# Kernel tuning notes

Hardware: AMD Instinct MI355X
Metric: run time of the kernel (lower is better)

The kernel has to match this reference:

```python
import jax, jax.numpy as jnp
import numpy as np

B, S, HID, H = 8, 128, 256, 4
DH = HID // H
FF = 4 * HID


def setup_inputs() -> dict:
    key = jax.random.key(0)
    ks = jax.random.split(key, 16)
    n = lambda i, shape: jax.random.normal(ks[i], shape, dtype=jnp.float32) * 0.02
    z = lambda shape: jnp.zeros(shape, dtype=jnp.float32)
    return dict(
        x=jax.random.normal(ks[0], (B, S, HID), dtype=jnp.float32),
        attention_mask=jnp.zeros((B, 1, S, S), dtype=jnp.float32),
        Wq=n(1, (HID, HID)), bq=z((HID,)),
        Wk=n(2, (HID, HID)), bk=z((HID,)),
        Wv=n(3, (HID, HID)), bv=z((HID,)),
        order_w=n(4, (2 * DH,)), order_b=z(()),
        dist_w=n(5, (2 * DH,)), dist_b=z(()),
        scalar=jax.random.normal(ks[6], (1,), dtype=jnp.float32),
        AWq=n(7, (HID, HID)), Abq=z((HID,)),
        AWk=n(8, (HID, HID)), Abk=z((HID,)),
        Wd=n(9, (HID, HID)), bd=z((HID,)),
        g1=jnp.ones((HID,), jnp.float32), beta1=z((HID,)),
        W1=n(10, (HID, FF)), b1=z((FF,)),
        W2=n(11, (FF, HID)), b2=z((HID,)),
        g2=jnp.ones((HID,), jnp.float32), beta2=z((HID,)),
    )


def _ln(t, g, b, eps=1e-12):
    m = t.mean(-1, keepdims=True)
    v = ((t - m) ** 2).mean(-1, keepdims=True)
    return (t - m) / jnp.sqrt(v + eps) * g + b


def _heads(t):
    # [B,S,HID] -> [B,H,S,DH]
    return t.reshape(B, S, H, DH).transpose(0, 2, 1, 3)


def reference(x, attention_mask, Wq, bq, Wk, bk, Wv, bv, order_w, order_b,
              dist_w, dist_b, scalar, AWq, Abq, AWk, Abk, Wd, bd,
              g1, beta1, W1, b1, W2, b2, g2, beta2):
    inv = 1.0 / jnp.sqrt(jnp.float32(DH))
    q = x @ Wq + bq
    k = x @ Wk + bk
    v = x @ Wv + bv
    qh, kh, vh = _heads(q), _heads(k), _heads(v)
    scores = jnp.einsum('bhqd,bhkd->bhqk', qh, kh)  # [B,H,S,S]

    # order/distance affines on concat(q_i, k_j): Linear(2*DH,1) decomposes into
    # per-token projections summed via broadcast (same math, no [B,H,S,S,2*DH] tensor)
    pr_order = jax.nn.sigmoid((qh @ order_w[:DH])[..., :, None]
                              + (kh @ order_w[DH:])[..., None, :] + order_b)
    gd_order = jnp.triu(jnp.ones((S, S), jnp.float32), k=1)
    err_order = (jnp.log(pr_order + 1e-24) * gd_order
                 + jnp.log(1.0 - pr_order + 1e-24) * (1.0 - gd_order))

    idx = jnp.arange(S)
    gd_dist = jnp.log(jnp.abs(idx[None, :] - idx[:, None]).astype(jnp.float32) + 1.0)
    pr_dist = ((qh @ dist_w[:DH])[..., :, None]
               + (kh @ dist_w[DH:])[..., None, :] + dist_b)
    err_dist = -jnp.square(gd_dist - pr_dist) * jnp.square(scalar[0]) * 0.5

    rich_scores = scores + err_order + err_dist
    softm = lambda s: jax.nn.softmax(s * inv + attention_mask, axis=-1)
    rich_probs = softm(rich_scores)
    origin_probs = softm(scores)

    # rich/calibrated combine ('fixed'): softmax(origin + 0.5 * rich)
    combined = jax.nn.softmax(origin_probs + 0.5 * rich_probs, axis=-1)

    # two-level attack attention on transformed mixed q/k
    aq, ak = _heads(q @ AWq + Abq), _heads(k @ AWk + Abk)
    attack_probs = softm(jnp.einsum('bhqd,bhkd->bhqk', aq, ak))
    final_probs = jax.nn.softmax(combined + 0.5 * attack_probs, axis=-1)

    ctx = jnp.einsum('bhqk,bhkd->bhqd', final_probs, vh)
    ctx = ctx.transpose(0, 2, 1, 3).reshape(B, S, HID)
    h = _ln(ctx @ Wd + bd + x, g1, beta1)
    f = jax.nn.gelu(h @ W1 + b1, approximate=False) @ W2 + b2
    return _ln(f + h, g2, beta2)
```

## Files before the change

kernel.cpp:

```cpp
#include <hip/hip_runtime.h>
#include <hip/hip_bf16.h>
#include <math.h>

#define B_  8
#define S_  128
#define HID_ 256
#define H_  4
#define DH_ 64
#define FF_ 1024
#define M_  (B_ * S_)

typedef _Float16 half_t;
typedef __attribute__((ext_vector_type(8))) _Float16 half8;
typedef __attribute__((ext_vector_type(4))) float floatx4;

enum { EP_F32 = 0, EP_F16 = 1, EP_F16B = 2, EP_GELU = 3, EP_PROJ = 4 };

__device__ __forceinline__ floatx4 mfma16(half8 a, half8 b, floatx4 c) {
    return __builtin_amdgcn_mfma_f32_16x16x32_f16(a, b, c, 0, 0, 0);
}

__device__ __forceinline__ float wred_sum(float v) {
#pragma unroll
    for (int o = 32; o >= 1; o >>= 1) v += __shfl_xor(v, o, 64);
    return v;
}
__device__ __forceinline__ float block_sum_256(float v, float* s4, int tid) {
    v = wred_sum(v);
    __syncthreads();
    if ((tid & 63) == 0) s4[tid >> 6] = v;
    __syncthreads();
    return s4[0] + s4[1] + s4[2] + s4[3];
}
__device__ __forceinline__ float qred_sum(float v) {
#pragma unroll
    for (int o = 1; o < 16; o <<= 1) v += __shfl_xor(v, o, 64);
    return v;
}
__device__ __forceinline__ void sm8(float (&v)[8]) {
    float s = 0.f;
#pragma unroll
    for (int j = 0; j < 8; ++j) { v[j] = __expf(v[j]); s += v[j]; }
    s = qred_sum(s);
    float r = 1.f / s;
#pragma unroll
    for (int j = 0; j < 8; ++j) v[j] *= r;
}

template<int EPI>
__device__ __forceinline__ void mgemm(
    const half_t* __restrict__ A, int ldA,
    const half_t* __restrict__ Bt, int ldB,
    int kLen, int m0, int n0,
    const float* __restrict__ bias,
    float* __restrict__ Cf, half_t* __restrict__ Ch, int ldC,
    const float* __restrict__ pw1, const float* __restrict__ pw2,
    float* __restrict__ po1, float* __restrict__ po2, int hsel)
{
    __shared__ half8 Asf[2][4][64];
    __shared__ half8 Bsf[2][4][64];

    const int tid = threadIdx.x;
    const int w = tid >> 6, l = tid & 63;
    const int sr = tid >> 2;
    const int sq = tid & 3;
    const int sdst = (sr & 15) | (sq << 4);
    const int smt = sr >> 4;
    const half_t* Ap = A + (size_t)(m0 + sr) * ldA + sq * 8;
    const half_t* Bp = Bt + (size_t)(n0 + sr) * ldB + sq * 8;

    half8 ra, rb;
    auto fetch = [&](int t) {
        ra = *(const half8*)(Ap + t * 32);
        rb = *(const half8*)(Bp + t * 32);
    };
    auto commit = [&](int buf) {
        Asf[buf][smt][sdst] = ra;
        Bsf[buf][smt][sdst] = rb;
    };

    floatx4 zero = {0.f, 0.f, 0.f, 0.f};
    floatx4 acc[4] = {zero, zero, zero, zero};
    const int kt = kLen >> 5;

    fetch(0);
    commit(0);
    __syncthreads();
    for (int t = 0; t < kt; ++t) {
        const bool more = (t + 1 < kt);
        if (more) fetch(t + 1);
        const int buf = t & 1;
        half8 a = Asf[buf][w][l];
        acc[0] = mfma16(a, Bsf[buf][0][l], acc[0]);
        acc[1] = mfma16(a, Bsf[buf][1][l], acc[1]);
        acc[2] = mfma16(a, Bsf[buf][2][l], acc[2]);
        acc[3] = mfma16(a, Bsf[buf][3][l], acc[3]);
        if (more) {
            commit((t + 1) & 1);
            __syncthreads();
        }
    }

    const int quad = l >> 4, lc = l & 15;
    const int rowb = m0 + w * 16 + quad * 4;
    float bvv[4] = {0.f, 0.f, 0.f, 0.f};
    if (EPI >= EP_F16B) {
#pragma unroll
        for (int nt = 0; nt < 4; ++nt) bvv[nt] = bias[n0 + nt * 16 + lc];
    }
    float pw1v[4], pw2v[4];
    if (EPI == EP_PROJ) {
#pragma unroll
        for (int nt = 0; nt < 4; ++nt) {
            pw1v[nt] = pw1[nt * 16 + lc];
            pw2v[nt] = pw2[nt * 16 + lc];
        }
    }
#pragma unroll
    for (int rr = 0; rr < 4; ++rr) {
        float ov[4];
#pragma unroll
        for (int nt = 0; nt < 4; ++nt) {
            float o = acc[nt][rr];
            if (EPI >= EP_F16B) o += bvv[nt];
            if (EPI == EP_GELU) o = 0.5f * o * (1.f + erff(o * 0.70710678118654752f));
            ov[nt] = o;
            const size_t ci = (size_t)(rowb + rr) * ldC + n0 + nt * 16 + lc;
            if (EPI == EP_F32) Cf[ci] = o;
            else Ch[ci] = (half_t)o;
        }
        if (EPI == EP_PROJ) {
            float po = ov[0] * pw1v[0] + ov[1] * pw1v[1] + ov[2] * pw1v[2] + ov[3] * pw1v[3];
            float pd = ov[0] * pw2v[0] + ov[1] * pw2v[1] + ov[2] * pw2v[2] + ov[3] * pw2v[3];
#pragma unroll
            for (int off = 1; off < 16; off <<= 1) {
                po += __shfl_xor(po, off, 64);
                pd += __shfl_xor(pd, off, 64);
            }
            if (lc == 0) {
                const int m = rowb + rr;
                const int idx = ((m >> 7) * H_ + hsel) * S_ + (m & 127);
                po1[idx] = po;
                po2[idx] = pd;
            }
        }
    }
}

__global__ __launch_bounds__(256) void prep_kernel(
    const float* __restrict__ x,
    const float* __restrict__ Wq, const float* __restrict__ Wk,
    const float* __restrict__ Wv, const float* __restrict__ Wd,
    const float* __restrict__ AWq, const float* __restrict__ AWk,
    const float* __restrict__ W1, const float* __restrict__ W2,
    half_t* __restrict__ x16, half_t* __restrict__ Wq16n, half_t* __restrict__ Wk16n,
    half_t* __restrict__ WqT, half_t* __restrict__ WkT, half_t* __restrict__ WvT,
    half_t* __restrict__ WdT, half_t* __restrict__ AWqT, half_t* __restrict__ AWkT,
    half_t* __restrict__ W1T, half_t* __restrict__ W2T)
{
    const int z = blockIdx.z, bx = blockIdx.x, by = blockIdx.y;
    const int tid = threadIdx.x;
    if (z < 3) {
        const float* src = (z == 0) ? x : (z == 1) ? Wq : Wk;
        half_t* dst = (z == 0) ? x16 : (z == 1) ? Wq16n : Wk16n;
        const int total = (z == 0) ? M_ * HID_ : HID_ * HID_;
        const int bid = by * 16 + bx;
        if (bid * 1024 < total) {
            const int base = bid * 1024 + tid * 4;
            float4 vv = *(const float4*)(src + base);
            dst[base + 0] = (half_t)vv.x;
            dst[base + 1] = (half_t)vv.y;
            dst[base + 2] = (half_t)vv.z;
            dst[base + 3] = (half_t)vv.w;
        }
        return;
    }
    const float* src; half_t* dst; int K, N, k0, n0;
    if (z <= 8) {
        const float* ins[6] = {Wq, Wk, Wv, Wd, AWq, AWk};
        half_t* outs[6] = {WqT, WkT, WvT, WdT, AWqT, AWkT};
        src = ins[z - 3]; dst = outs[z - 3];
        K = 256; N = 256; k0 = bx * 64; n0 = by * 64;
        if (bx >= 4 || by >= 4) return;
    } else if (z == 9) {
        src = W1; dst = W1T; K = 256; N = 1024;
        k0 = bx * 64; n0 = by * 64;
        if (bx >= 4) return;
    } else {
        src = W2; dst = W2T; K = 1024; N = 256;
        k0 = by * 64; n0 = bx * 64;
        if (bx >= 4) return;
    }
    __shared__ half_t tl[64][72];
    const int r = tid >> 2, c0 = (tid & 3) * 16;
#pragma unroll 4
    for (int i = 0; i < 16; ++i)
        tl[c0 + i][r] = (half_t)src[(size_t)(k0 + r) * N + n0 + c0 + i];
    __syncthreads();
#pragma unroll 4
    for (int i = 0; i < 16; ++i)
        dst[(size_t)(n0 + r) * K + k0 + c0 + i] = tl[r][c0 + i];
}

__global__ __launch_bounds__(256) void compose_mfma(
    const half_t* __restrict__ AWqT, const half_t* __restrict__ AWkT,
    const half_t* __restrict__ Wq16n, const half_t* __restrict__ Wk16n,
    const float* __restrict__ AWq, const float* __restrict__ AWk,
    const float* __restrict__ bq, const float* __restrict__ bk,
    const float* __restrict__ Abq, const float* __restrict__ Abk,
    half_t* __restrict__ WcqT, half_t* __restrict__ WckT,
    float* __restrict__ bcq, float* __restrict__ bck)
{
    const int z = blockIdx.z;
    if (blockIdx.y < 4) {
        const half_t* A = z ? AWkT : AWqT;
        const half_t* Bt = z ? Wk16n : Wq16n;
        half_t* C = z ? WckT : WcqT;
        mgemm<EP_F16>(A, HID_, Bt, HID_, HID_, blockIdx.y * 64, blockIdx.x * 64,
                      nullptr, nullptr, C, HID_, nullptr, nullptr, nullptr, nullptr, 0);
    } else {
        __shared__ float red[4][64];
        const float* bsrc = z ? bk : bq;
        const float* AW   = z ? AWk : AWq;
        const float* Ab   = z ? Abk : Abq;
        float* bco        = z ? bck : bcq;
        int t = threadIdx.x, l = t & 63, kc = t >> 6;
        int n = blockIdx.x * 64 + l;
        float p = 0.f;
#pragma unroll 8
        for (int kk = 0; kk < 64; ++kk) {
            int k = kc * 64 + kk;
            p = fmaf(bsrc[k], AW[(size_t)k * HID_ + n], p);
        }
        red[kc][l] = p;
        __syncthreads();
        if (kc == 0)
            bco[n] = red[0][l] + red[1][l] + red[2][l] + red[3][l] + Ab[n];
    }
}

__global__ __launch_bounds__(256) void xgemm5(
    const half_t* __restrict__ x16,
    const half_t* __restrict__ WqT, const float* __restrict__ bq,
    const half_t* __restrict__ WkT, const float* __restrict__ bk,
    const half_t* __restrict__ WvT, const float* __restrict__ bv,
    const half_t* __restrict__ WcqT, const float* __restrict__ bcq,
    const half_t* __restrict__ WckT, const float* __restrict__ bck,
    const float* __restrict__ order_w, const float* __restrict__ dist_w,
    half_t* __restrict__ q16, half_t* __restrict__ k16, half_t* __restrict__ v16,
    half_t* __restrict__ aq16, half_t* __restrict__ ak16,
    float* __restrict__ qoA, float* __restrict__ qdA,
    float* __restrict__ koA, float* __restrict__ kdA)
{
    const int z = blockIdx.z;
    const int m0 = blockIdx.y * 64, n0 = blockIdx.x * 64;
    if (z == 0)
        mgemm<EP_PROJ>(x16, HID_, WqT, HID_, HID_, m0, n0, bq, nullptr, q16, HID_,
                       order_w, dist_w, qoA, qdA, blockIdx.x);
    else if (z == 1)
        mgemm<EP_PROJ>(x16, HID_, WkT, HID_, HID_, m0, n0, bk, nullptr, k16, HID_,
                       order_w + DH_, dist_w + DH_, koA, kdA, blockIdx.x);
    else if (z == 2)
        mgemm<EP_F16B>(x16, HID_, WvT, HID_, HID_, m0, n0, bv, nullptr, v16, HID_,
                       nullptr, nullptr, nullptr, nullptr, 0);
    else if (z == 3)
        mgemm<EP_F16B>(x16, HID_, WcqT, HID_, HID_, m0, n0, bcq, nullptr, aq16, HID_,
                       nullptr, nullptr, nullptr, nullptr, 0);
    else
        mgemm<EP_F16B>(x16, HID_, WckT, HID_, HID_, m0, n0, bck, nullptr, ak16, HID_,
                       nullptr, nullptr, nullptr, nullptr, 0);
}

__global__ __launch_bounds__(64) void attn_fused(
    const half_t* __restrict__ q16, const half_t* __restrict__ k16,
    const half_t* __restrict__ v16, const half_t* __restrict__ aq16,
    const half_t* __restrict__ ak16,
    const float* __restrict__ qoA, const float* __restrict__ qdA,
    const float* __restrict__ koA, const float* __restrict__ kdA,
    const float* __restrict__ mask,
    const float* __restrict__ order_b_p, const float* __restrict__ dist_b_p,
    const float* __restrict__ scalar_p,
    half_t* __restrict__ ctx16)
{
    __shared__ half8 Qf[2][64], AQf[2][64];
    __shared__ half8 Kf[2][8][64], AKf[2][8][64];
    __shared__ half_t Vt[64][136];
    __shared__ half_t Pm[16][136];

    const int l = threadIdx.x;
    const int quad = l >> 4, lc = l & 15;
    const int bh = blockIdx.x >> 3, rt = blockIdx.x & 7;
    const int b = bh >> 2, h = bh & 3;
    const size_t hoff = (size_t)b * S_ * HID_ + h * DH_;

#pragma unroll
    for (int u = 0; u < 2; ++u) {
        int idx = u * 64 + l;
        int r = idx >> 3, c = idx & 7;
        size_t g = hoff + (size_t)(rt * 16 + r) * HID_ + c * 8;
        int kt = c >> 2, sl = r | ((c & 3) << 4);
        Qf[kt][sl]  = *(const half8*)(q16 + g);
        AQf[kt][sl] = *(const half8*)(aq16 + g);
    }
#pragma unroll
    for (int u = 0; u < 16; ++u) {
        int idx = u * 64 + l;
        int j = idx >> 3, c = idx & 7;
        size_t g = hoff + (size_t)j * HID_ + c * 8;
        int kt = c >> 2, jt = j >> 4, sl = (j & 15) | ((c & 3) << 4);
        Kf[kt][jt][sl]  = *(const half8*)(k16 + g);
        AKf[kt][jt][sl] = *(const half8*)(ak16 + g);
    }
#pragma unroll
    for (int u = 0; u < 16; ++u) {
        int j = (u >> 3) * 64 + l;
        int c = u & 7;
        half8 vv = *(const half8*)(v16 + hoff + (size_t)j * HID_ + c * 8);
#pragma unroll
        for (int e = 0; e < 8; ++e) Vt[c * 8 + e][j] = vv[e];
    }
    __syncthreads();

    floatx4 zero = {0.f, 0.f, 0.f, 0.f};
    floatx4 accS[8], accA[8];
#pragma unroll
    for (int jt = 0; jt < 8; ++jt) { accS[jt] = zero; accA[jt] = zero; }
#pragma unroll
    for (int kt = 0; kt < 2; ++kt) {
        half8 a0 = Qf[kt][l];
        half8 a1 = AQf[kt][l];
#pragma unroll
        for (int jt = 0; jt < 8; ++jt) {
            accS[jt] = mfma16(a0, Kf[kt][jt][l], accS[jt]);
            accA[jt] = mfma16(a1, AKf[kt][jt][l], accA[jt]);
        }
    }

    const float ob = order_b_p[0], db = dist_b_p[0];
    const float scl = scalar_p[0];
    const float s2 = scl * scl;
    const float inv = 0.125f;
    float kov[8], kdv[8];
#pragma unroll
    for (int jt = 0; jt < 8; ++jt) {
        kov[jt] = koA[bh * S_ + jt * 16 + lc];
        kdv[jt] = kdA[bh * S_ + jt * 16 + lc];
    }
#pragma unroll
    for (int reg = 0; reg < 4; ++reg) {
        const int il = quad * 4 + reg;
        const int i  = rt * 16 + il;
        float qo = qoA[bh * S_ + i], qd = qdA[bh * S_ + i];
        const float* mrow = mask + ((size_t)(b * S_ + i)) * S_;
        float mk[8], lg[8], as_[8];
#pragma unroll
        for (int jt = 0; jt < 8; ++jt) {
            mk[jt] = mrow[jt * 16 + lc];
            lg[jt] = accS[jt][reg];
            as_[jt] = accA[jt][reg];
        }
        float p0[8];
#pragma unroll
        for (int jt = 0; jt < 8; ++jt) p0[jt] = lg[jt] * inv + mk[jt];
        sm8(p0);
        float p1[8];
#pragma unroll
        for (int jt = 0; jt < 8; ++jt) {
            int j = jt * 16 + lc;
            float pr = 1.f / (1.f + __expf(-(qo + kov[jt] + ob)));
            float sel = (j > i) ? pr : 1.f - pr;
            float erro = __logf(sel + 1e-24f);
            float gd = __logf(fabsf((float)(j - i)) + 1.f);
            float dd = gd - (qd + kdv[jt] + db);
            p1[jt] = (lg[jt] + erro - 0.5f * dd * dd * s2) * inv + mk[jt];
        }
        sm8(p1);
#pragma unroll
        for (int jt = 0; jt < 8; ++jt) p0[jt] += 0.5f * p1[jt];
        sm8(p0);
#pragma unroll
        for (int jt = 0; jt < 8; ++jt) p1[jt] = as_[jt] * inv + mk[jt];
        sm8(p1);
#pragma unroll
        for (int jt = 0; jt < 8; ++jt) p0[jt] += 0.5f * p1[jt];
        sm8(p0);
#pragma unroll
        for (int jt = 0; jt < 8; ++jt) Pm[il][jt * 16 + lc] = (half_t)p0[jt];
    }
    __syncthreads();

    half8 pa_[4];
#pragma unroll
    for (int kt = 0; kt < 4; ++kt)
        pa_[kt] = *(const half8*)&Pm[lc][kt * 32 + quad * 8];
    floatx4 apv[4];
#pragma unroll
    for (int nt = 0; nt < 4; ++nt) apv[nt] = zero;
#pragma unroll
    for (int nt = 0; nt < 4; ++nt) {
#pragma unroll
        for (int kt = 0; kt < 4; ++kt) {
            half8 vf = *(const half8*)&Vt[nt * 16 + lc][kt * 32 + quad * 8];
            apv[nt] = mfma16(pa_[kt], vf, apv[nt]);
        }
    }
#pragma unroll
    for (int nt = 0; nt < 4; ++nt) {
#pragma unroll
        for (int reg = 0; reg < 4; ++reg) {
            int i = rt * 16 + quad * 4 + reg;
            ctx16[hoff + (size_t)i * HID_ + nt * 16 + lc] = (half_t)apv[nt][reg];
        }
    }
}

__global__ __launch_bounds__(256) void dense_mfma(
    const half_t* __restrict__ ctx16, const half_t* __restrict__ WdT,
    float* __restrict__ dn)
{
    mgemm<EP_F32>(ctx16, HID_, WdT, HID_, HID_, blockIdx.y * 64, blockIdx.x * 64,
                  nullptr, dn, nullptr, HID_, nullptr, nullptr, nullptr, nullptr, 0);
}

__global__ __launch_bounds__(256) void ff1_mfma(
    const half_t* __restrict__ h16, const half_t* __restrict__ W1T,
    const float* __restrict__ b1, half_t* __restrict__ f116)
{
    mgemm<EP_GELU>(h16, HID_, W1T, HID_, HID_, blockIdx.y * 64, blockIdx.x * 64,
                   b1, nullptr, f116, FF_, nullptr, nullptr, nullptr, nullptr, 0);
}

__global__ __launch_bounds__(256) void ff2_mfma(
    const half_t* __restrict__ f116, const half_t* __restrict__ W2T,
    float* __restrict__ p0, float* __restrict__ p1,
    float* __restrict__ p2, float* __restrict__ p3)
{
    const int z = blockIdx.z;
    float* C = (z == 0) ? p0 : (z == 1) ? p1 : (z == 2) ? p2 : p3;
    mgemm<EP_F32>(f116 + z * 256, FF_, W2T + z * 256, FF_, 256,
                  blockIdx.y * 64, blockIdx.x * 64,
                  nullptr, C, nullptr, HID_, nullptr, nullptr, nullptr, nullptr, 0);
}

__global__ __launch_bounds__(256) void ln1_kernel(
    const float* __restrict__ dn, const float* __restrict__ bd,
    const float* __restrict__ x,
    const float* __restrict__ g1, const float* __restrict__ beta1,
    float* __restrict__ h32, half_t* __restrict__ h16)
{
    __shared__ float s4[4];
    const int row = blockIdx.x;
    const int n = threadIdx.x;
    const size_t idx = (size_t)row * HID_ + n;
    float val = dn[idx] + bd[n] + x[idx];
    float mean = block_sum_256(val, s4, n) * (1.f / HID_);
    float dv = val - mean;
    float var = block_sum_256(dv * dv, s4, n) * (1.f / HID_);
    float r = dv * rsqrtf(var + 1e-12f) * g1[n] + beta1[n];
    h32[idx] = r;
    h16[idx] = (half_t)r;
}

__global__ __launch_bounds__(256) void ln2_kernel(
    const float* __restrict__ p0, const float* __restrict__ p1,
    const float* __restrict__ p2, const float* __restrict__ p3,
    const float* __restrict__ b2, const float* __restrict__ h32,
    const float* __restrict__ g2, const float* __restrict__ beta2,
    float* __restrict__ out)
{
    __shared__ float s4[4];
    const int row = blockIdx.x;
    const int n = threadIdx.x;
    const size_t idx = (size_t)row * HID_ + n;
    float val = p0[idx] + p1[idx] + p2[idx] + p3[idx] + b2[n] + h32[idx];
    float mean = block_sum_256(val, s4, n) * (1.f / HID_);
    float dv = val - mean;
    float var = block_sum_256(dv * dv, s4, n) * (1.f / HID_);
    out[idx] = dv * rsqrtf(var + 1e-12f) * g2[n] + beta2[n];
}

extern "C" void kernel_launch(void* const* d_in, const int* in_sizes, int n_in,
                              void* d_out, int out_size, void* d_ws, size_t ws_size,
                              hipStream_t stream) {
    const float* x        = (const float*)d_in[0];
    const float* mask     = (const float*)d_in[1];
    const float* Wq       = (const float*)d_in[2];
    const float* bq       = (const float*)d_in[3];
    const float* Wk       = (const float*)d_in[4];
    const float* bk       = (const float*)d_in[5];
    const float* Wv       = (const float*)d_in[6];
    const float* bv       = (const float*)d_in[7];
    const float* order_w  = (const float*)d_in[8];
    const float* order_b  = (const float*)d_in[9];
    const float* dist_w   = (const float*)d_in[10];
    const float* dist_b   = (const float*)d_in[11];
    const float* scalar   = (const float*)d_in[12];
    const float* AWq      = (const float*)d_in[13];
    const float* Abq      = (const float*)d_in[14];
    const float* AWk      = (const float*)d_in[15];
    const float* Abk      = (const float*)d_in[16];
    const float* Wd       = (const float*)d_in[17];
    const float* bd       = (const float*)d_in[18];
    const float* g1       = (const float*)d_in[19];
    const float* beta1    = (const float*)d_in[20];
    const float* W1       = (const float*)d_in[21];
    const float* b1       = (const float*)d_in[22];
    const float* W2       = (const float*)d_in[23];
    const float* b2       = (const float*)d_in[24];
    const float* g2       = (const float*)d_in[25];
    const float* beta2    = (const float*)d_in[26];

    float* ws = (float*)d_ws;
    size_t off = 0;
    auto afl = [&](size_t n) { float* p = ws + off; off += n; return p; };
    auto ahf = [&](size_t nh) { half_t* p = (half_t*)(ws + off); off += nh / 2; return p; };

    half_t* x16   = ahf(M_ * HID_);
    half_t* Wq16n = ahf(HID_ * HID_);
    half_t* Wk16n = ahf(HID_ * HID_);
    half_t* WqT   = ahf(HID_ * HID_);
    half_t* WkT   = ahf(HID_ * HID_);
    half_t* WvT   = ahf(HID_ * HID_);
    half_t* WdT   = ahf(HID_ * HID_);
    half_t* AWqT  = ahf(HID_ * HID_);
    half_t* AWkT  = ahf(HID_ * HID_);
    half_t* W1T   = ahf(HID_ * FF_);
    half_t* W2T   = ahf(HID_ * FF_);
    half_t* WcqT  = ahf(HID_ * HID_);
    half_t* WckT  = ahf(HID_ * HID_);
    half_t* q16   = ahf(M_ * HID_);
    half_t* k16   = ahf(M_ * HID_);
    half_t* v16   = ahf(M_ * HID_);
    half_t* aq16  = ahf(M_ * HID_);
    half_t* ak16  = ahf(M_ * HID_);
    half_t* ctx16 = ahf(M_ * HID_);
    half_t* h16   = ahf(M_ * HID_);
    half_t* f116  = ahf(M_ * FF_);
    float* dnb  = afl(M_ * HID_);
    float* hb32 = afl(M_ * HID_);
    float* pf0  = afl(M_ * HID_);
    float* pf1  = afl(M_ * HID_);
    float* pf2  = afl(M_ * HID_);
    float* pf3  = afl(M_ * HID_);
    float* bcq  = afl(256);
    float* bck  = afl(256);
    float* qoA  = afl(B_ * H_ * S_);
    float* qdA  = afl(B_ * H_ * S_);
    float* koA  = afl(B_ * H_ * S_);
    float* kdA  = afl(B_ * H_ * S_);

    prep_kernel<<<dim3(16, 16, 11), 256, 0, stream>>>(
        x, Wq, Wk, Wv, Wd, AWq, AWk, W1, W2,
        x16, Wq16n, Wk16n, WqT, WkT, WvT, WdT, AWqT, AWkT, W1T, W2T);
    compose_mfma<<<dim3(4, 5, 2), 256, 0, stream>>>(
        AWqT, AWkT, Wq16n, Wk16n, AWq, AWk, bq, bk, Abq, Abk, WcqT, WckT, bcq, bck);
    xgemm5<<<dim3(4, 16, 5), 256, 0, stream>>>(
        x16, WqT, bq, WkT, bk, WvT, bv, WcqT, bcq, WckT, bck, order_w, dist_w,
        q16, k16, v16, aq16, ak16, qoA, qdA, koA, kdA);
    attn_fused<<<256, 64, 0, stream>>>(
        q16, k16, v16, aq16, ak16, qoA, qdA, koA, kdA,
        mask, order_b, dist_b, scalar, ctx16);
    dense_mfma<<<dim3(4, 16), 256, 0, stream>>>(ctx16, WdT, dnb);
    ln1_kernel<<<M_, 256, 0, stream>>>(dnb, bd, x, g1, beta1, hb32, h16);
    ff1_mfma<<<dim3(16, 16), 256, 0, stream>>>(h16, W1T, b1, f116);
    ff2_mfma<<<dim3(4, 16, 4), 256, 0, stream>>>(f116, W2T, pf0, pf1, pf2, pf3);
    ln2_kernel<<<M_, 256, 0, stream>>>(pf0, pf1, pf2, pf3, b2, hb32, g2, beta2, (float*)d_out);
}
```

Baseline: 162.7 us.

## Fuse all stages into one persistent megakernel with global barriers

```diff
diff --git a/kernel.cpp b/kernel.cpp
--- a/kernel.cpp
+++ b/kernel.cpp
@@ -1,5 +1,4 @@
 #include <hip/hip_runtime.h>
-#include <hip/hip_bf16.h>
 #include <math.h>
 
 #define B_  8
@@ -9,6 +8,7 @@
 #define DH_ 64
 #define FF_ 1024
 #define M_  (B_ * S_)
+#define NBLK 256
 
 typedef _Float16 half_t;
 typedef __attribute__((ext_vector_type(8))) _Float16 half8;
@@ -20,18 +20,19 @@
     return __builtin_amdgcn_mfma_f32_16x16x32_f16(a, b, c, 0, 0, 0);
 }
 
-__device__ __forceinline__ float wred_sum(float v) {
-#pragma unroll
-    for (int o = 32; o >= 1; o >>= 1) v += __shfl_xor(v, o, 64);
-    return v;
-}
-__device__ __forceinline__ float block_sum_256(float v, float* s4, int tid) {
-    v = wred_sum(v);
-    __syncthreads();
-    if ((tid & 63) == 0) s4[tid >> 6] = v;
-    __syncthreads();
-    return s4[0] + s4[1] + s4[2] + s4[3];
-}
+__device__ __forceinline__ void gbar(int* bar, int phase) {
+    __syncthreads();
+    if (threadIdx.x == 0) {
+        __threadfence();
+        __hip_atomic_fetch_add(bar, 1, __ATOMIC_ACQ_REL, __HIP_MEMORY_SCOPE_AGENT);
+        while (__hip_atomic_load(bar, __ATOMIC_ACQUIRE, __HIP_MEMORY_SCOPE_AGENT)
+               < phase * NBLK)
+            __builtin_amdgcn_s_sleep(8);
+        __threadfence();
+    }
+    __syncthreads();
+}
+
 __device__ __forceinline__ float qred_sum(float v) {
 #pragma unroll
     for (int o = 1; o < 16; o <<= 1) v += __shfl_xor(v, o, 64);
@@ -49,6 +50,7 @@
 
 template<int EPI>
 __device__ __forceinline__ void mgemm(
+    half8 (&Asf)[2][4][64], half8 (&Bsf)[2][4][64],
     const half_t* __restrict__ A, int ldA,
     const half_t* __restrict__ Bt, int ldB,
     int kLen, int m0, int n0,
@@ -57,9 +59,6 @@
     const float* __restrict__ pw1, const float* __restrict__ pw2,
     float* __restrict__ po1, float* __restrict__ po2, int hsel)
 {
-    __shared__ half8 Asf[2][4][64];
-    __shared__ half8 Bsf[2][4][64];
-
     const int tid = threadIdx.x;
     const int w = tid >> 6, l = tid & 63;
     const int sr = tid >> 2;
@@ -147,336 +146,372 @@
     }
 }
 
-__global__ __launch_bounds__(256) void prep_kernel(
-    const float* __restrict__ x,
-    const float* __restrict__ Wq, const float* __restrict__ Wk,
-    const float* __restrict__ Wv, const float* __restrict__ Wd,
-    const float* __restrict__ AWq, const float* __restrict__ AWk,
-    const float* __restrict__ W1, const float* __restrict__ W2,
-    half_t* __restrict__ x16, half_t* __restrict__ Wq16n, half_t* __restrict__ Wk16n,
-    half_t* __restrict__ WqT, half_t* __restrict__ WkT, half_t* __restrict__ WvT,
-    half_t* __restrict__ WdT, half_t* __restrict__ AWqT, half_t* __restrict__ AWkT,
-    half_t* __restrict__ W1T, half_t* __restrict__ W2T)
-{
-    const int z = blockIdx.z, bx = blockIdx.x, by = blockIdx.y;
-    const int tid = threadIdx.x;
-    if (z < 3) {
-        const float* src = (z == 0) ? x : (z == 1) ? Wq : Wk;
-        half_t* dst = (z == 0) ? x16 : (z == 1) ? Wq16n : Wk16n;
-        const int total = (z == 0) ? M_ * HID_ : HID_ * HID_;
-        const int bid = by * 16 + bx;
-        if (bid * 1024 < total) {
-            const int base = bid * 1024 + tid * 4;
-            float4 vv = *(const float4*)(src + base);
-            dst[base + 0] = (half_t)vv.x;
-            dst[base + 1] = (half_t)vv.y;
-            dst[base + 2] = (half_t)vv.z;
-            dst[base + 3] = (half_t)vv.w;
-        }
+
+struct MegaParams {
+    const float *x, *mask;
+    const float *Wq, *bq, *Wk, *bk, *Wv, *bv;
+    const float *order_w, *order_b, *dist_w, *dist_b, *scalar;
+    const float *AWq, *Abq, *AWk, *Abk, *Wd, *bd, *g1, *beta1;
+    const float *W1, *b1, *W2, *b2, *g2, *beta2;
+    half_t *x16, *WqT, *WkT, *WvT, *WdT, *AWqT, *AWkT, *W1T, *W2T;
+    half_t *q16, *k16, *v16, *aq16, *ak16, *ctx16;
+    float *qoA, *qdA, *koA, *kdA;
+    float *out;
+};
+
+union SMem {
+    struct { half8 Asf[2][4][64]; half8 Bsf[2][4][64]; } g;
+    struct { half_t tl[64][72]; } p;
+    struct {
+        half8 Kf[2][8][64]; half8 AKf[2][8][64];
+        half_t Vt[64][136]; half_t Pm[16][136];
+    } a;
+    struct {
+        half8 Af[8][64];
+        float hS[16][257];
+        half_t h16L[16][264];
+        half_t f116L[16][1032];
+    } t;
+};
+
+#define NJOBS_PREP 480
+__device__ __forceinline__ void prep_job(const MegaParams& P, SMem& sm, int j, int tid) {
+    if (j < 256) {
+        const int base = j * 1024 + tid * 4;
+        float4 vv = *(const float4*)(P.x + base);
+        P.x16[base + 0] = (half_t)vv.x;
+        P.x16[base + 1] = (half_t)vv.y;
+        P.x16[base + 2] = (half_t)vv.z;
+        P.x16[base + 3] = (half_t)vv.w;
         return;
     }
+    int t = j - 256;
     const float* src; half_t* dst; int K, N, k0, n0;
-    if (z <= 8) {
-        const float* ins[6] = {Wq, Wk, Wv, Wd, AWq, AWk};
-        half_t* outs[6] = {WqT, WkT, WvT, WdT, AWqT, AWkT};
-        src = ins[z - 3]; dst = outs[z - 3];
-        K = 256; N = 256; k0 = bx * 64; n0 = by * 64;
-        if (bx >= 4 || by >= 4) return;
-    } else if (z == 9) {
-        src = W1; dst = W1T; K = 256; N = 1024;
-        k0 = bx * 64; n0 = by * 64;
-        if (bx >= 4) return;
+    if (t < 96) {
+        int m = t >> 4, q = t & 15;
+        const float* ins[6] = {P.Wq, P.Wk, P.Wv, P.Wd, P.AWq, P.AWk};
+        half_t* outs[6] = {P.WqT, P.WkT, P.WvT, P.WdT, P.AWqT, P.AWkT};
+        src = ins[m]; dst = outs[m]; K = 256; N = 256;
+        k0 = (q & 3) * 64; n0 = (q >> 2) * 64;
+    } else if (t < 160) {
+        int q = t - 96; src = P.W1; dst = P.W1T; K = 256; N = 1024;
+        k0 = (q & 3) * 64; n0 = (q >> 2) * 64;
     } else {
-        src = W2; dst = W2T; K = 1024; N = 256;
-        k0 = by * 64; n0 = bx * 64;
-        if (bx >= 4) return;
-    }
-    __shared__ half_t tl[64][72];
+        int q = t - 160; src = P.W2; dst = P.W2T; K = 1024; N = 256;
+        k0 = (q >> 2) * 64; n0 = (q & 3) * 64;
+    }
+    __syncthreads();
     const int r = tid >> 2, c0 = (tid & 3) * 16;
 #pragma unroll 4
     for (int i = 0; i < 16; ++i)
-        tl[c0 + i][r] = (half_t)src[(size_t)(k0 + r) * N + n0 + c0 + i];
+        sm.p.tl[c0 + i][r] = (half_t)src[(size_t)(k0 + r) * N + n0 + c0 + i];
     __syncthreads();
 #pragma unroll 4
     for (int i = 0; i < 16; ++i)
-        dst[(size_t)(n0 + r) * K + k0 + c0 + i] = tl[r][c0 + i];
-}
-
-__global__ __launch_bounds__(256) void compose_mfma(
-    const half_t* __restrict__ AWqT, const half_t* __restrict__ AWkT,
-    const half_t* __restrict__ Wq16n, const half_t* __restrict__ Wk16n,
-    const float* __restrict__ AWq, const float* __restrict__ AWk,
-    const float* __restrict__ bq, const float* __restrict__ bk,
-    const float* __restrict__ Abq, const float* __restrict__ Abk,
-    half_t* __restrict__ WcqT, half_t* __restrict__ WckT,
-    float* __restrict__ bcq, float* __restrict__ bck)
-{
-    const int z = blockIdx.z;
-    if (blockIdx.y < 4) {
-        const half_t* A = z ? AWkT : AWqT;
-        const half_t* Bt = z ? Wk16n : Wq16n;
-        half_t* C = z ? WckT : WcqT;
-        mgemm<EP_F16>(A, HID_, Bt, HID_, HID_, blockIdx.y * 64, blockIdx.x * 64,
-                      nullptr, nullptr, C, HID_, nullptr, nullptr, nullptr, nullptr, 0);
-    } else {
-        __shared__ float red[4][64];
-        const float* bsrc = z ? bk : bq;
-        const float* AW   = z ? AWk : AWq;
-        const float* Ab   = z ? Abk : Abq;
-        float* bco        = z ? bck : bcq;
-        int t = threadIdx.x, l = t & 63, kc = t >> 6;
-        int n = blockIdx.x * 64 + l;
-        float p = 0.f;
-#pragma unroll 8
-        for (int kk = 0; kk < 64; ++kk) {
-            int k = kc * 64 + kk;
-            p = fmaf(bsrc[k], AW[(size_t)k * HID_ + n], p);
-        }
-        red[kc][l] = p;
-        __syncthreads();
-        if (kc == 0)
-            bco[n] = red[0][l] + red[1][l] + red[2][l] + red[3][l] + Ab[n];
-    }
-}
-
-__global__ __launch_bounds__(256) void xgemm5(
-    const half_t* __restrict__ x16,
-    const half_t* __restrict__ WqT, const float* __restrict__ bq,
-    const half_t* __restrict__ WkT, const float* __restrict__ bk,
-    const half_t* __restrict__ WvT, const float* __restrict__ bv,
-    const half_t* __restrict__ WcqT, const float* __restrict__ bcq,
-    const half_t* __restrict__ WckT, const float* __restrict__ bck,
-    const float* __restrict__ order_w, const float* __restrict__ dist_w,
-    half_t* __restrict__ q16, half_t* __restrict__ k16, half_t* __restrict__ v16,
-    half_t* __restrict__ aq16, half_t* __restrict__ ak16,
-    float* __restrict__ qoA, float* __restrict__ qdA,
-    float* __restrict__ koA, float* __restrict__ kdA)
-{
-    const int z = blockIdx.z;
-    const int m0 = blockIdx.y * 64, n0 = blockIdx.x * 64;
+        dst[(size_t)(n0 + r) * K + k0 + c0 + i] = sm.p.tl[r][c0 + i];
+}
+
+__device__ __forceinline__ void qkv_job(const MegaParams& P, SMem& sm, int j) {
+    const int z = j >> 6, q = j & 63;
+    const int m0 = (q >> 2) * 64, n0 = (q & 3) * 64, bx = q & 3;
     if (z == 0)
-        mgemm<EP_PROJ>(x16, HID_, WqT, HID_, HID_, m0, n0, bq, nullptr, q16, HID_,
-                       order_w, dist_w, qoA, qdA, blockIdx.x);
+        mgemm<EP_PROJ>(sm.g.Asf, sm.g.Bsf, P.x16, HID_, P.WqT, HID_, HID_, m0, n0,
+                       P.bq, nullptr, P.q16, HID_, P.order_w, P.dist_w, P.qoA, P.qdA, bx);
     else if (z == 1)
-        mgemm<EP_PROJ>(x16, HID_, WkT, HID_, HID_, m0, n0, bk, nullptr, k16, HID_,
-                       order_w + DH_, dist_w + DH_, koA, kdA, blockIdx.x);
-    else if (z == 2)
-        mgemm<EP_F16B>(x16, HID_, WvT, HID_, HID_, m0, n0, bv, nullptr, v16, HID_,
-                       nullptr, nullptr, nullptr, nullptr, 0);
-    else if (z == 3)
-        mgemm<EP_F16B>(x16, HID_, WcqT, HID_, HID_, m0, n0, bcq, nullptr, aq16, HID_,
-                       nullptr, nullptr, nullptr, nullptr, 0);
+        mgemm<EP_PROJ>(sm.g.Asf, sm.g.Bsf, P.x16, HID_, P.WkT, HID_, HID_, m0, n0,
+                       P.bk, nullptr, P.k16, HID_, P.order_w + DH_, P.dist_w + DH_,
+                       P.koA, P.kdA, bx);
     else
-        mgemm<EP_F16B>(x16, HID_, WckT, HID_, HID_, m0, n0, bck, nullptr, ak16, HID_,
-                       nullptr, nullptr, nullptr, nullptr, 0);
-}
-
-__global__ __launch_bounds__(64) void attn_fused(
-    const half_t* __restrict__ q16, const half_t* __restrict__ k16,
-    const half_t* __restrict__ v16, const half_t* __restrict__ aq16,
-    const half_t* __restrict__ ak16,
-    const float* __restrict__ qoA, const float* __restrict__ qdA,
-    const float* __restrict__ koA, const float* __restrict__ kdA,
-    const float* __restrict__ mask,
-    const float* __restrict__ order_b_p, const float* __restrict__ dist_b_p,
-    const float* __restrict__ scalar_p,
-    half_t* __restrict__ ctx16)
-{
-    __shared__ half8 Qf[2][64], AQf[2][64];
-    __shared__ half8 Kf[2][8][64], AKf[2][8][64];
-    __shared__ half_t Vt[64][136];
-    __shared__ half_t Pm[16][136];
-
-    const int l = threadIdx.x;
+        mgemm<EP_F16B>(sm.g.Asf, sm.g.Bsf, P.x16, HID_, P.WvT, HID_, HID_, m0, n0,
+                       P.bv, nullptr, P.v16, HID_, nullptr, nullptr, nullptr, nullptr, 0);
+}
+
+__device__ __forceinline__ void aqak_job(const MegaParams& P, SMem& sm, int j) {
+    const int z = j >> 6, q = j & 63;
+    const int m0 = (q >> 2) * 64, n0 = (q & 3) * 64;
+    if (z == 0)
+        mgemm<EP_F16B>(sm.g.Asf, sm.g.Bsf, P.q16, HID_, P.AWqT, HID_, HID_, m0, n0,
+                       P.Abq, nullptr, P.aq16, HID_, nullptr, nullptr, nullptr, nullptr, 0);
+    else
+        mgemm<EP_F16B>(sm.g.Asf, sm.g.Bsf, P.k16, HID_, P.AWkT, HID_, HID_, m0, n0,
+                       P.Abk, nullptr, P.ak16, HID_, nullptr, nullptr, nullptr, nullptr, 0);
+}
+
+__device__ __forceinline__ void attn_job(const MegaParams& P, SMem& sm, int blk, int tid) {
+    const int bh = blk >> 3, rt = blk & 7;
+    const int b = bh >> 2, h = bh & 3;
+    const size_t hoff = (size_t)b * S_ * HID_ + (size_t)h * DH_;
+    const int l = tid & 63, w = tid >> 6;
     const int quad = l >> 4, lc = l & 15;
-    const int bh = blockIdx.x >> 3, rt = blockIdx.x & 7;
-    const int b = bh >> 2, h = bh & 3;
-    const size_t hoff = (size_t)b * S_ * HID_ + h * DH_;
-
-#pragma unroll
-    for (int u = 0; u < 2; ++u) {
-        int idx = u * 64 + l;
-        int r = idx >> 3, c = idx & 7;
-        size_t g = hoff + (size_t)(rt * 16 + r) * HID_ + c * 8;
-        int kt = c >> 2, sl = r | ((c & 3) << 4);
-        Qf[kt][sl]  = *(const half8*)(q16 + g);
-        AQf[kt][sl] = *(const half8*)(aq16 + g);
-    }
-#pragma unroll
-    for (int u = 0; u < 16; ++u) {
-        int idx = u * 64 + l;
+
+#pragma unroll
+    for (int u = 0; u < 4; ++u) {
+        int idx = u * 256 + tid;
         int j = idx >> 3, c = idx & 7;
         size_t g = hoff + (size_t)j * HID_ + c * 8;
         int kt = c >> 2, jt = j >> 4, sl = (j & 15) | ((c & 3) << 4);
-        Kf[kt][jt][sl]  = *(const half8*)(k16 + g);
-        AKf[kt][jt][sl] = *(const half8*)(ak16 + g);
-    }
-#pragma unroll
-    for (int u = 0; u < 16; ++u) {
-        int j = (u >> 3) * 64 + l;
-        int c = u & 7;
-        half8 vv = *(const half8*)(v16 + hoff + (size_t)j * HID_ + c * 8);
-#pragma unroll
-        for (int e = 0; e < 8; ++e) Vt[c * 8 + e][j] = vv[e];
-    }
-    __syncthreads();
-
-    floatx4 zero = {0.f, 0.f, 0.f, 0.f};
-    floatx4 accS[8], accA[8];
-#pragma unroll
-    for (int jt = 0; jt < 8; ++jt) { accS[jt] = zero; accA[jt] = zero; }
-#pragma unroll
-    for (int kt = 0; kt < 2; ++kt) {
-        half8 a0 = Qf[kt][l];
-        half8 a1 = AQf[kt][l];
+        sm.a.Kf[kt][jt][sl]  = *(const half8*)(P.k16 + g);
+        sm.a.AKf[kt][jt][sl] = *(const half8*)(P.ak16 + g);
+    }
+#pragma unroll
+    for (int u = 0; u < 4; ++u) {
+        int idx = u * 256 + tid;
+        int j = idx >> 3, c = idx & 7;
+        half8 vv = *(const half8*)(P.v16 + hoff + (size_t)j * HID_ + c * 8);
+#pragma unroll
+        for (int e = 0; e < 8; ++e) sm.a.Vt[c * 8 + e][j] = vv[e];
+    }
+    __syncthreads();
+
+    if (w == 0) {
+        half8 qf[2], aqf[2];
+#pragma unroll
+        for (int kt = 0; kt < 2; ++kt) {
+            size_t g = hoff + (size_t)(rt * 16 + lc) * HID_ + kt * 32 + quad * 8;
+            qf[kt]  = *(const half8*)(P.q16 + g);
+            aqf[kt] = *(const half8*)(P.aq16 + g);
+        }
+        floatx4 zero = {0.f, 0.f, 0.f, 0.f};
+        floatx4 accS[8], accA[8];
+#pragma unroll
+        for (int jt = 0; jt < 8; ++jt) { accS[jt] = zero; accA[jt] = zero; }
+#pragma unroll
+        for (int kt = 0; kt < 2; ++kt) {
+#pragma unroll
+            for (int jt = 0; jt < 8; ++jt) {
+                accS[jt] = mfma16(qf[kt], sm.a.Kf[kt][jt][l], accS[jt]);
+                accA[jt] = mfma16(aqf[kt], sm.a.AKf[kt][jt][l], accA[jt]);
+            }
+        }
+
+        const float ob = P.order_b[0], db = P.dist_b[0];
+        const float scl = P.scalar[0];
+        const float s2 = scl * scl;
+        const float inv = 0.125f;
+        float kov[8], kdv[8];
 #pragma unroll
         for (int jt = 0; jt < 8; ++jt) {
-            accS[jt] = mfma16(a0, Kf[kt][jt][l], accS[jt]);
-            accA[jt] = mfma16(a1, AKf[kt][jt][l], accA[jt]);
-        }
-    }
-
-    const float ob = order_b_p[0], db = dist_b_p[0];
-    const float scl = scalar_p[0];
-    const float s2 = scl * scl;
-    const float inv = 0.125f;
-    float kov[8], kdv[8];
-#pragma unroll
-    for (int jt = 0; jt < 8; ++jt) {
-        kov[jt] = koA[bh * S_ + jt * 16 + lc];
-        kdv[jt] = kdA[bh * S_ + jt * 16 + lc];
-    }
-#pragma unroll
-    for (int reg = 0; reg < 4; ++reg) {
-        const int il = quad * 4 + reg;
-        const int i  = rt * 16 + il;
-        float qo = qoA[bh * S_ + i], qd = qdA[bh * S_ + i];
-        const float* mrow = mask + ((size_t)(b * S_ + i)) * S_;
-        float mk[8], lg[8], as_[8];
-#pragma unroll
-        for (int jt = 0; jt < 8; ++jt) {
-            mk[jt] = mrow[jt * 16 + lc];
-            lg[jt] = accS[jt][reg];
-            as_[jt] = accA[jt][reg];
-        }
-        float p0[8];
-#pragma unroll
-        for (int jt = 0; jt < 8; ++jt) p0[jt] = lg[jt] * inv + mk[jt];
-        sm8(p0);
-        float p1[8];
-#pragma unroll
-        for (int jt = 0; jt < 8; ++jt) {
-            int j = jt * 16 + lc;
-            float pr = 1.f / (1.f + __expf(-(qo + kov[jt] + ob)));
-            float sel = (j > i) ? pr : 1.f - pr;
-            float erro = __logf(sel + 1e-24f);
-            float gd = __logf(fabsf((float)(j - i)) + 1.f);
-            float dd = gd - (qd + kdv[jt] + db);
-            p1[jt] = (lg[jt] + erro - 0.5f * dd * dd * s2) * inv + mk[jt];
-        }
-        sm8(p1);
-#pragma unroll
-        for (int jt = 0; jt < 8; ++jt) p0[jt] += 0.5f * p1[jt];
-        sm8(p0);
-#pragma unroll
-        for (int jt = 0; jt < 8; ++jt) p1[jt] = as_[jt] * inv + mk[jt];
-        sm8(p1);
-#pragma unroll
-        for (int jt = 0; jt < 8; ++jt) p0[jt] += 0.5f * p1[jt];
-        sm8(p0);
-#pragma unroll
-        for (int jt = 0; jt < 8; ++jt) Pm[il][jt * 16 + lc] = (half_t)p0[jt];
-    }
-    __syncthreads();
-
-    half8 pa_[4];
-#pragma unroll
-    for (int kt = 0; kt < 4; ++kt)
-        pa_[kt] = *(const half8*)&Pm[lc][kt * 32 + quad * 8];
-    floatx4 apv[4];
-#pragma unroll
-    for (int nt = 0; nt < 4; ++nt) apv[nt] = zero;
-#pragma unroll
-    for (int nt = 0; nt < 4; ++nt) {
-#pragma unroll
-        for (int kt = 0; kt < 4; ++kt) {
-            half8 vf = *(const half8*)&Vt[nt * 16 + lc][kt * 32 + quad * 8];
-            apv[nt] = mfma16(pa_[kt], vf, apv[nt]);
-        }
-    }
-#pragma unroll
-    for (int nt = 0; nt < 4; ++nt) {
+            kov[jt] = P.koA[bh * S_ + jt * 16 + lc];
+            kdv[jt] = P.kdA[bh * S_ + jt * 16 + lc];
+        }
 #pragma unroll
         for (int reg = 0; reg < 4; ++reg) {
-            int i = rt * 16 + quad * 4 + reg;
-            ctx16[hoff + (size_t)i * HID_ + nt * 16 + lc] = (half_t)apv[nt][reg];
-        }
-    }
-}
-
-__global__ __launch_bounds__(256) void dense_mfma(
-    const half_t* __restrict__ ctx16, const half_t* __restrict__ WdT,
-    float* __restrict__ dn)
-{
-    mgemm<EP_F32>(ctx16, HID_, WdT, HID_, HID_, blockIdx.y * 64, blockIdx.x * 64,
-                  nullptr, dn, nullptr, HID_, nullptr, nullptr, nullptr, nullptr, 0);
-}
-
-__global__ __launch_bounds__(256) void ff1_mfma(
-    const half_t* __restrict__ h16, const half_t* __restrict__ W1T,
-    const float* __restrict__ b1, half_t* __restrict__ f116)
-{
-    mgemm<EP_GELU>(h16, HID_, W1T, HID_, HID_, blockIdx.y * 64, blockIdx.x * 64,
-                   b1, nullptr, f116, FF_, nullptr, nullptr, nullptr, nullptr, 0);
-}
-
-__global__ __launch_bounds__(256) void ff2_mfma(
-    const half_t* __restrict__ f116, const half_t* __restrict__ W2T,
-    float* __restrict__ p0, float* __restrict__ p1,
-    float* __restrict__ p2, float* __restrict__ p3)
-{
-    const int z = blockIdx.z;
-    float* C = (z == 0) ? p0 : (z == 1) ? p1 : (z == 2) ? p2 : p3;
-    mgemm<EP_F32>(f116 + z * 256, FF_, W2T + z * 256, FF_, 256,
-                  blockIdx.y * 64, blockIdx.x * 64,
-                  nullptr, C, nullptr, HID_, nullptr, nullptr, nullptr, nullptr, 0);
-}
-
-__global__ __launch_bounds__(256) void ln1_kernel(
-    const float* __restrict__ dn, const float* __restrict__ bd,
-    const float* __restrict__ x,
-    const float* __restrict__ g1, const float* __restrict__ beta1,
-    float* __restrict__ h32, half_t* __restrict__ h16)
-{
-    __shared__ float s4[4];
-    const int row = blockIdx.x;
-    const int n = threadIdx.x;
-    const size_t idx = (size_t)row * HID_ + n;
-    float val = dn[idx] + bd[n] + x[idx];
-    float mean = block_sum_256(val, s4, n) * (1.f / HID_);
-    float dv = val - mean;
-    float var = block_sum_256(dv * dv, s4, n) * (1.f / HID_);
-    float r = dv * rsqrtf(var + 1e-12f) * g1[n] + beta1[n];
-    h32[idx] = r;
-    h16[idx] = (half_t)r;
-}
-
-__global__ __launch_bounds__(256) void ln2_kernel(
-    const float* __restrict__ p0, const float* __restrict__ p1,
-    const float* __restrict__ p2, const float* __restrict__ p3,
-    const float* __restrict__ b2, const float* __restrict__ h32,
-    const float* __restrict__ g2, const float* __restrict__ beta2,
-    float* __restrict__ out)
-{
-    __shared__ float s4[4];
-    const int row = blockIdx.x;
-    const int n = threadIdx.x;
-    const size_t idx = (size_t)row * HID_ + n;
-    float val = p0[idx] + p1[idx] + p2[idx] + p3[idx] + b2[n] + h32[idx];
-    float mean = block_sum_256(val, s4, n) * (1.f / HID_);
-    float dv = val - mean;
-    float var = block_sum_256(dv * dv, s4, n) * (1.f / HID_);
-    out[idx] = dv * rsqrtf(var + 1e-12f) * g2[n] + beta2[n];
+            const int il = quad * 4 + reg;
+            const int i  = rt * 16 + il;
+            float qo = P.qoA[bh * S_ + i], qd = P.qdA[bh * S_ + i];
+            const float* mrow = P.mask + ((size_t)(b * S_ + i)) * S_;
+            float mk[8], lg[8], as_[8];
+#pragma unroll
+            for (int jt = 0; jt < 8; ++jt) {
+                mk[jt] = mrow[jt * 16 + lc];
+                lg[jt] = accS[jt][reg];
+                as_[jt] = accA[jt][reg];
+            }
+            float p0[8];
+#pragma unroll
+            for (int jt = 0; jt < 8; ++jt) p0[jt] = lg[jt] * inv + mk[jt];
+            sm8(p0);
+            float p1[8];
+#pragma unroll
+            for (int jt = 0; jt < 8; ++jt) {
+                int j = jt * 16 + lc;
+                float pr = 1.f / (1.f + __expf(-(qo + kov[jt] + ob)));
+                float sel = (j > i) ? pr : 1.f - pr;
+                float erro = __logf(sel + 1e-24f);
+                float gd = __logf(fabsf((float)(j - i)) + 1.f);
+                float dd = gd - (qd + kdv[jt] + db);
+                p1[jt] = (lg[jt] + erro - 0.5f * dd * dd * s2) * inv + mk[jt];
+            }
+            sm8(p1);
+#pragma unroll
+            for (int jt = 0; jt < 8; ++jt) p0[jt] += 0.5f * p1[jt];
+            sm8(p0);
+#pragma unroll
+            for (int jt = 0; jt < 8; ++jt) p1[jt] = as_[jt] * inv + mk[jt];
+            sm8(p1);
+#pragma unroll
+            for (int jt = 0; jt < 8; ++jt) p0[jt] += 0.5f * p1[jt];
+            sm8(p0);
+#pragma unroll
+            for (int jt = 0; jt < 8; ++jt) sm.a.Pm[il][jt * 16 + lc] = (half_t)p0[jt];
+        }
+    }
+    __syncthreads();
+
+    if (w == 0) {
+        half8 pa_[4];
+#pragma unroll
+        for (int kt = 0; kt < 4; ++kt)
+            pa_[kt] = *(const half8*)&sm.a.Pm[lc][kt * 32 + quad * 8];
+        floatx4 zero = {0.f, 0.f, 0.f, 0.f};
+        floatx4 apv[4] = {zero, zero, zero, zero};
+#pragma unroll
+        for (int nt = 0; nt < 4; ++nt) {
+#pragma unroll
+            for (int kt = 0; kt < 4; ++kt) {
+                half8 vf = *(const half8*)&sm.a.Vt[nt * 16 + lc][kt * 32 + quad * 8];
+                apv[nt] = mfma16(pa_[kt], vf, apv[nt]);
+            }
+        }
+#pragma unroll
+        for (int nt = 0; nt < 4; ++nt) {
+#pragma unroll
+            for (int reg = 0; reg < 4; ++reg) {
+                int i = rt * 16 + quad * 4 + reg;
+                P.ctx16[hoff + (size_t)i * HID_ + nt * 16 + lc] = (half_t)apv[nt][reg];
+            }
+        }
+    }
+}
+
+__device__ __forceinline__ void tail_job(const MegaParams& P, SMem& sm, int blk, int tid) {
+    const int r0 = blk * 16;
+    const int w = tid >> 6, l = tid & 63;
+    const int quad = l >> 4, lc = l & 15;
+    const floatx4 zero = {0.f, 0.f, 0.f, 0.f};
+
+#pragma unroll
+    for (int u = 0; u < 2; ++u) {
+        int idx = u * 256 + tid;
+        int row = idx >> 5, c = idx & 31;
+        sm.t.Af[c >> 2][row | ((c & 3) << 4)] =
+            *(const half8*)(P.ctx16 + (size_t)(r0 + row) * HID_ + c * 8);
+    }
+    __syncthreads();
+
+    {
+        const int n0 = w * 64;
+        floatx4 acc[4] = {zero, zero, zero, zero};
+#pragma unroll
+        for (int kt = 0; kt < 8; ++kt) {
+            half8 a = sm.t.Af[kt][l];
+#pragma unroll
+            for (int nt = 0; nt < 4; ++nt) {
+                half8 b = *(const half8*)(P.WdT + (size_t)(n0 + nt * 16 + lc) * HID_
+                                          + kt * 32 + quad * 8);
+                acc[nt] = mfma16(a, b, acc[nt]);
+            }
+        }
+#pragma unroll
+        for (int nt = 0; nt < 4; ++nt)
+#pragma unroll
+            for (int rr = 0; rr < 4; ++rr) {
+                int row = quad * 4 + rr, col = n0 + nt * 16 + lc;
+                sm.t.hS[row][col] = acc[nt][rr] + P.bd[col]
+                                  + P.x[(size_t)(r0 + row) * HID_ + col];
+            }
+    }
+    __syncthreads();
+
+    {
+        const int row = tid >> 4, jj = tid & 15;
+        float s = 0.f;
+#pragma unroll
+        for (int i = 0; i < 16; ++i) s += sm.t.hS[row][i * 16 + jj];
+#pragma unroll
+        for (int o = 1; o < 16; o <<= 1) s += __shfl_xor(s, o, 64);
+        float mean = s * (1.f / 256.f);
+        float vs = 0.f;
+#pragma unroll
+        for (int i = 0; i < 16; ++i) { float d = sm.t.hS[row][i * 16 + jj] - mean; vs += d * d; }
+#pragma unroll
+        for (int o = 1; o < 16; o <<= 1) vs += __shfl_xor(vs, o, 64);
+        float rs = rsqrtf(vs * (1.f / 256.f) + 1e-12f);
+#pragma unroll
+        for (int i = 0; i < 16; ++i) {
+            int col = i * 16 + jj;
+            float v = (sm.t.hS[row][col] - mean) * rs * P.g1[col] + P.beta1[col];
+            sm.t.hS[row][col] = v;
+            sm.t.h16L[row][col] = (half_t)v;
+        }
+    }
+    __syncthreads();
+
+#pragma unroll
+    for (int nb = 0; nb < 4; ++nb) {
+        const int n0 = w * 256 + nb * 64;
+        floatx4 acc[4] = {zero, zero, zero, zero};
+#pragma unroll
+        for (int kt = 0; kt < 8; ++kt) {
+            half8 a = *(const half8*)&sm.t.h16L[l & 15][kt * 32 + quad * 8];
+#pragma unroll
+            for (int nt = 0; nt < 4; ++nt) {
+                half8 b = *(const half8*)(P.W1T + (size_t)(n0 + nt * 16 + lc) * HID_
+                                          + kt * 32 + quad * 8);
+                acc[nt] = mfma16(a, b, acc[nt]);
+            }
+        }
+#pragma unroll
+        for (int nt = 0; nt < 4; ++nt)
+#pragma unroll
+            for (int rr = 0; rr < 4; ++rr) {
+                int row = quad * 4 + rr, col = n0 + nt * 16 + lc;
+                float o = acc[nt][rr] + P.b1[col];
+                o = 0.5f * o * (1.f + erff(o * 0.70710678118654752f));
+                sm.t.f116L[row][col] = (half_t)o;
+            }
+    }
+    __syncthreads();
+
+    {
+        const int n0 = w * 64;
+        floatx4 acc[4] = {zero, zero, zero, zero};
+#pragma unroll
+        for (int kt = 0; kt < 32; ++kt) {
+            half8 a = *(const half8*)&sm.t.f116L[l & 15][kt * 32 + quad * 8];
+#pragma unroll
+            for (int nt = 0; nt < 4; ++nt) {
+                half8 b = *(const half8*)(P.W2T + (size_t)(n0 + nt * 16 + lc) * FF_
+                                          + kt * 32 + quad * 8);
+                acc[nt] = mfma16(a, b, acc[nt]);
+            }
+        }
+#pragma unroll
+        for (int nt = 0; nt < 4; ++nt)
+#pragma unroll
+            for (int rr = 0; rr < 4; ++rr) {
+                int row = quad * 4 + rr, col = n0 + nt * 16 + lc;
+                sm.t.hS[row][col] = acc[nt][rr] + P.b2[col] + sm.t.hS[row][col];
+            }
+    }
+    __syncthreads();
+
+    {
+        const int row = tid >> 4, jj = tid & 15;
+        float s = 0.f;
+#pragma unroll
+        for (int i = 0; i < 16; ++i) s += sm.t.hS[row][i * 16 + jj];
+#pragma unroll
+        for (int o = 1; o < 16; o <<= 1) s += __shfl_xor(s, o, 64);
+        float mean = s * (1.f / 256.f);
+        float vs = 0.f;
+#pragma unroll
+        for (int i = 0; i < 16; ++i) { float d = sm.t.hS[row][i * 16 + jj] - mean; vs += d * d; }
+#pragma unroll
+        for (int o = 1; o < 16; o <<= 1) vs += __shfl_xor(vs, o, 64);
+        float rs = rsqrtf(vs * (1.f / 256.f) + 1e-12f);
+#pragma unroll
+        for (int i = 0; i < 16; ++i) {
+            int col = i * 16 + jj;
+            P.out[(size_t)(r0 + row) * HID_ + col] =
+                (sm.t.hS[row][col] - mean) * rs * P.g2[col] + P.beta2[col];
+        }
+    }
+}
+
+__global__ __launch_bounds__(256) void mega_kernel(MegaParams P, int* bar) {
+    __shared__ SMem sm;
+    const int blk = blockIdx.x, tid = threadIdx.x;
+
+    for (int j = blk; j < NJOBS_PREP; j += NBLK) prep_job(P, sm, j, tid);
+    gbar(bar, 1);
+    if (blk < 192) qkv_job(P, sm, blk);
+    gbar(bar, 2);
+    if (blk < 128) aqak_job(P, sm, blk);
+    gbar(bar, 3);
+    attn_job(P, sm, blk, tid);
+    gbar(bar, 4);
+    if (blk < 64) tail_job(P, sm, blk, tid);
 }
 
 extern "C" void kernel_launch(void* const* d_in, const int* in_sizes, int n_in,
@@ -511,13 +546,12 @@
     const float* beta2    = (const float*)d_in[26];
 
     float* ws = (float*)d_ws;
-    size_t off = 0;
+    int* bar = (int*)ws;
+    size_t off = 64;
+    auto ahf = [&](size_t nh) { half_t* p = (half_t*)(ws + off); off += nh / 2; return p; };
     auto afl = [&](size_t n) { float* p = ws + off; off += n; return p; };
-    auto ahf = [&](size_t nh) { half_t* p = (half_t*)(ws + off); off += nh / 2; return p; };
 
     half_t* x16   = ahf(M_ * HID_);
-    half_t* Wq16n = ahf(HID_ * HID_);
-    half_t* Wk16n = ahf(HID_ * HID_);
     half_t* WqT   = ahf(HID_ * HID_);
     half_t* WkT   = ahf(HID_ * HID_);
     half_t* WvT   = ahf(HID_ * HID_);
@@ -526,43 +560,32 @@
     half_t* AWkT  = ahf(HID_ * HID_);
     half_t* W1T   = ahf(HID_ * FF_);
     half_t* W2T   = ahf(HID_ * FF_);
-    half_t* WcqT  = ahf(HID_ * HID_);
-    half_t* WckT  = ahf(HID_ * HID_);
     half_t* q16   = ahf(M_ * HID_);
     half_t* k16   = ahf(M_ * HID_);
     half_t* v16   = ahf(M_ * HID_);
     half_t* aq16  = ahf(M_ * HID_);
     half_t* ak16  = ahf(M_ * HID_);
     half_t* ctx16 = ahf(M_ * HID_);
-    half_t* h16   = ahf(M_ * HID_);
-    half_t* f116  = ahf(M_ * FF_);
-    float* dnb  = afl(M_ * HID_);
-    float* hb32 = afl(M_ * HID_);
-    float* pf0  = afl(M_ * HID_);
-    float* pf1  = afl(M_ * HID_);
-    float* pf2  = afl(M_ * HID_);
-    float* pf3  = afl(M_ * HID_);
-    float* bcq  = afl(256);
-    float* bck  = afl(256);
     float* qoA  = afl(B_ * H_ * S_);
     float* qdA  = afl(B_ * H_ * S_);
     float* koA  = afl(B_ * H_ * S_);
     float* kdA  = afl(B_ * H_ * S_);
 
-    prep_kernel<<<dim3(16, 16, 11), 256, 0, stream>>>(
-        x, Wq, Wk, Wv, Wd, AWq, AWk, W1, W2,
-        x16, Wq16n, Wk16n, WqT, WkT, WvT, WdT, AWqT, AWkT, W1T, W2T);
-    compose_mfma<<<dim3(4, 5, 2), 256, 0, stream>>>(
-        AWqT, AWkT, Wq16n, Wk16n, AWq, AWk, bq, bk, Abq, Abk, WcqT, WckT, bcq, bck);
-    xgemm5<<<dim3(4, 16, 5), 256, 0, stream>>>(
-        x16, WqT, bq, WkT, bk, WvT, bv, WcqT, bcq, WckT, bck, order_w, dist_w,
-        q16, k16, v16, aq16, ak16, qoA, qdA, koA, kdA);
-    attn_fused<<<256, 64, 0, stream>>>(
-        q16, k16, v16, aq16, ak16, qoA, qdA, koA, kdA,
-        mask, order_b, dist_b, scalar, ctx16);
-    dense_mfma<<<dim3(4, 16), 256, 0, stream>>>(ctx16, WdT, dnb);
-    ln1_kernel<<<M_, 256, 0, stream>>>(dnb, bd, x, g1, beta1, hb32, h16);
-    ff1_mfma<<<dim3(16, 16), 256, 0, stream>>>(h16, W1T, b1, f116);
-    ff2_mfma<<<dim3(4, 16, 4), 256, 0, stream>>>(f116, W2T, pf0, pf1, pf2, pf3);
-    ln2_kernel<<<M_, 256, 0, stream>>>(pf0, pf1, pf2, pf3, b2, hb32, g2, beta2, (float*)d_out);
-}
+    MegaParams mp;
+    mp.x = x; mp.mask = mask;
+    mp.Wq = Wq; mp.bq = bq; mp.Wk = Wk; mp.bk = bk; mp.Wv = Wv; mp.bv = bv;
+    mp.order_w = order_w; mp.order_b = order_b;
+    mp.dist_w = dist_w; mp.dist_b = dist_b; mp.scalar = scalar;
+    mp.AWq = AWq; mp.Abq = Abq; mp.AWk = AWk; mp.Abk = Abk;
+    mp.Wd = Wd; mp.bd = bd; mp.g1 = g1; mp.beta1 = beta1;
+    mp.W1 = W1; mp.b1 = b1; mp.W2 = W2; mp.b2 = b2; mp.g2 = g2; mp.beta2 = beta2;
+    mp.x16 = x16; mp.WqT = WqT; mp.WkT = WkT; mp.WvT = WvT; mp.WdT = WdT;
+    mp.AWqT = AWqT; mp.AWkT = AWkT; mp.W1T = W1T; mp.W2T = W2T;
+    mp.q16 = q16; mp.k16 = k16; mp.v16 = v16; mp.aq16 = aq16; mp.ak16 = ak16;
+    mp.ctx16 = ctx16;
+    mp.qoA = qoA; mp.qdA = qdA; mp.koA = koA; mp.kdA = kdA;
+    mp.out = (float*)d_out;
+
+    hipMemsetAsync(bar, 0, 256, stream);
+    mega_kernel<<<NBLK, 256, 0, stream>>>(mp, bar);
+}
```

Measured after the change: 312.8 us. 92.2% more time.
